# Optimization experiments

Measured on AMD Instinct MI355X. Metric: run time of the kernel, lower is better.

Reference implementation:

```python
import jax, jax.numpy as jnp
import numpy as np

L = 5          # num_layer
D = 128        # emb_dim
F = 16         # raw node/edge feature dim
N = 50000      # nodes
E = 800000     # edges
BN_EPS = 1e-5


def _bn(z, g, b):
    # BatchNorm1d forward with batch statistics (training-mode math)
    m = z.mean(axis=0)
    v = z.var(axis=0)
    return (z - m) * jax.lax.rsqrt(v + BN_EPS) * g + b


def setup_inputs() -> dict:
    key = jax.random.key(0)
    ks = jax.random.split(key, 8)
    s = lambda *sh: 0.05  # weight scale
    return {
        "x": jax.random.normal(ks[0], (N, F), jnp.float32),
        "edge_index": jax.random.randint(ks[1], (2, E), 0, N, jnp.int32),
        "edge_attr": jax.random.normal(ks[2], (E, F), jnp.float32),
        "W_node": jax.random.normal(ks[3], (F, D), jnp.float32) * 0.05,
        "b_node": jnp.zeros((D,), jnp.float32),
        "We": jax.random.normal(ks[4], (L, F, D), jnp.float32) * 0.05,
        "be": jnp.zeros((L, D), jnp.float32),
        "eps_gin": jnp.zeros((L,), jnp.float32),
        "W1": jax.random.normal(ks[5], (L, D, 2 * D), jnp.float32) * 0.05,
        "b1": jnp.zeros((L, 2 * D), jnp.float32),
        "g1": jnp.ones((L, 2 * D), jnp.float32),
        "beta1": jnp.zeros((L, 2 * D), jnp.float32),
        "W2": jax.random.normal(ks[6], (L, 2 * D, D), jnp.float32) * 0.05,
        "b2": jnp.zeros((L, D), jnp.float32),
        "g_bn": jnp.ones((L, D), jnp.float32),
        "beta_bn": jnp.zeros((L, D), jnp.float32),
    }


def reference(x, edge_index, edge_attr, W_node, b_node, We, be, eps_gin,
              W1, b1, g1, beta1, W2, b2, g_bn, beta_bn):
    src, dst = edge_index[0], edge_index[1]
    n = x.shape[0]
    h = x @ W_node + b_node                       # node encoder: [N, D]
    for l in range(L):
        e = edge_attr @ We[l] + be[l]             # edge encoder: [E, D]
        msg = jax.nn.relu(h[src] + e)             # gather + message
        agg = jax.ops.segment_sum(msg, dst, num_segments=n)  # scatter-add
        z = (1.0 + eps_gin[l]) * h + agg
        z = _bn(z @ W1[l] + b1[l], g1[l], beta1[l])  # GIN MLP hidden
        z = jax.nn.relu(z)
        z = z @ W2[l] + b2[l]                     # GIN MLP out: [N, D]
        z = _bn(z, g_bn[l], beta_bn[l])           # per-layer BatchNorm
        if l < L - 1:
            z = jax.nn.relu(z)                    # dropout is identity (p=0)
        h = z + h                                 # residual
    return h                                      # JK = 'last'
```

## Files before the change

kernel.cpp:

```cpp
#include <hip/hip_runtime.h>
#include <hip/hip_bf16.h>

#define NN 50000
#define EE 800000
#define DD 128
#define FF 16
#define LL 5
#define NPART 3125

typedef __attribute__((ext_vector_type(8))) short bf16x8;
typedef __attribute__((ext_vector_type(4))) float f32x4;

__device__ __forceinline__ unsigned short f2bf(float f) {
    union { float f; unsigned int u; } v; v.f = f;
    unsigned int u = v.u;
    unsigned int r = (u + 0x7fffu + ((u >> 16) & 1u)) >> 16;
    return (unsigned short)r;
}
__device__ __forceinline__ float bf2f(unsigned short s) {
    union { unsigned int u; float f; } v; v.u = ((unsigned int)s) << 16;
    return v.f;
}

__global__ void k_node_enc(const float* __restrict__ x, const float* __restrict__ Wn,
                           const float* __restrict__ bn, float* __restrict__ h)
{
    const int t = blockIdx.x * 256 + threadIdx.x;
    const int i = t >> 7, d = t & 127;
    const float4* x4 = (const float4*)(x + (size_t)i * 16);
    float4 a0 = x4[0], a1 = x4[1], a2 = x4[2], a3 = x4[3];
    float acc = bn[d];
    acc += a0.x*Wn[0*128+d] + a0.y*Wn[1*128+d] + a0.z*Wn[2*128+d] + a0.w*Wn[3*128+d];
    acc += a1.x*Wn[4*128+d] + a1.y*Wn[5*128+d] + a1.z*Wn[6*128+d] + a1.w*Wn[7*128+d];
    acc += a2.x*Wn[8*128+d] + a2.y*Wn[9*128+d] + a2.z*Wn[10*128+d] + a2.w*Wn[11*128+d];
    acc += a3.x*Wn[12*128+d] + a3.y*Wn[13*128+d] + a3.z*Wn[14*128+d] + a3.w*Wn[15*128+d];
    h[t] = acc;
}

__global__ void k_count(const int* __restrict__ ei, int* __restrict__ counts)
{
    const int e = blockIdx.x * 256 + threadIdx.x;
    atomicAdd(&counts[ei[EE + e]], 1);
}

__global__ __launch_bounds__(1024) void k_scan(int* __restrict__ counts, int* __restrict__ row_ptr)
{
    __shared__ int wsum[16];
    __shared__ int carry;
    const int tid = threadIdx.x, lane = tid & 63, w = tid >> 6;
    if (tid == 0) carry = 0;
    __syncthreads();
    for (int base = 0; base < NN; base += 1024) {
        const int i = base + tid;
        const int v = (i < NN) ? counts[i] : 0;
        int x = v;
        #pragma unroll
        for (int off = 1; off < 64; off <<= 1) {
            const int t = __shfl_up(x, off);
            if (lane >= off) x += t;
        }
        if (lane == 63) wsum[w] = x;
        __syncthreads();
        int woff = 0, total = 0;
        #pragma unroll
        for (int j = 0; j < 16; ++j) { const int s = wsum[j]; total += s; if (j < w) woff += s; }
        const int ex = carry + woff + x - v;
        if (i < NN) { row_ptr[i] = ex; counts[i] = ex; }
        __syncthreads();
        if (tid == 0) carry += total;
        __syncthreads();
    }
    if (tid == 0) row_ptr[NN] = carry;
}

__global__ void k_fill(const int* __restrict__ ei, int* __restrict__ cursor, int2* __restrict__ eidsrc)
{
    const int e = blockIdx.x * 256 + threadIdx.x;
    const int d = ei[EE + e];
    const int p = atomicAdd(&cursor[d], 1);
    eidsrc[p] = make_int2(e, ei[e]);
}

__global__ void k_pack(const float* __restrict__ W1, const float* __restrict__ W2,
                       unsigned short* __restrict__ Wp1, unsigned short* __restrict__ Wp2)
{
    int t = blockIdx.x * 256 + threadIdx.x;
    const int total = LL * 32768;
    if (t < total) {
        const int l = t >> 15, r = t & 32767;
        const int j = r & 7, lane = (r >> 3) & 63, kt = (r >> 9) & 3, nt = r >> 11;
        const int k = kt * 32 + (lane >> 4) * 8 + j;
        const int n = nt * 16 + (lane & 15);
        Wp1[t] = f2bf(W1[(size_t)l * 32768 + k * 256 + n]);
    } else {
        t -= total;
        const int l = t >> 15, r = t & 32767;
        const int j = r & 7, lane = (r >> 3) & 63, kt = (r >> 9) & 7, nt = r >> 12;
        const int k = kt * 32 + (lane >> 4) * 8 + j;
        const int n = nt * 16 + (lane & 15);
        Wp2[t] = f2bf(W2[(size_t)l * 32768 + k * 128 + n]);
    }
}

__global__ __launch_bounds__(256) void k_agg(
    const float* __restrict__ h, const float* __restrict__ ea,
    const float* __restrict__ We_l, const float* __restrict__ be_l,
    const int* __restrict__ row_ptr, const int2* __restrict__ eidsrc,
    float* __restrict__ agg)
{
    const int wv = threadIdx.x >> 6;
    const int v  = blockIdx.x * 4 + wv;
    const int lane = threadIdx.x & 63;
    const int c2 = lane * 2;
    float2 w[16];
    #pragma unroll
    for (int f = 0; f < 16; ++f) w[f] = *(const float2*)(We_l + f * 128 + c2);
    const float2 bed = *(const float2*)(be_l + c2);
    const int kbeg = __builtin_amdgcn_readfirstlane(row_ptr[v]);
    const int kend = __builtin_amdgcn_readfirstlane(row_ptr[v + 1]);
    float2 acc0 = {0.f, 0.f}, acc1 = {0.f, 0.f}, acc2 = {0.f, 0.f}, acc3 = {0.f, 0.f};

#define EDGE_DOT(eidx_, hs_, out_) do {                                        \
        const float4* p_ = (const float4*)(ea + (size_t)(eidx_) * 16);         \
        const float4 a0_ = p_[0], a1_ = p_[1], a2_ = p_[2], a3_ = p_[3];       \
        float ex_ = bed.x, ey_ = bed.y;                                        \
        ex_ += a0_.x*w[0].x  + a0_.y*w[1].x  + a0_.z*w[2].x  + a0_.w*w[3].x;   \
        ey_ += a0_.x*w[0].y  + a0_.y*w[1].y  + a0_.z*w[2].y  + a0_.w*w[3].y;   \
        ex_ += a1_.x*w[4].x  + a1_.y*w[5].x  + a1_.z*w[6].x  + a1_.w*w[7].x;   \
        ey_ += a1_.x*w[4].y  + a1_.y*w[5].y  + a1_.z*w[6].y  + a1_.w*w[7].y;   \
        ex_ += a2_.x*w[8].x  + a2_.y*w[9].x  + a2_.z*w[10].x + a2_.w*w[11].x;  \
        ey_ += a2_.x*w[8].y  + a2_.y*w[9].y  + a2_.z*w[10].y + a2_.w*w[11].y;  \
        ex_ += a3_.x*w[12].x + a3_.y*w[13].x + a3_.z*w[14].x + a3_.w*w[15].x;  \
        ey_ += a3_.x*w[12].y + a3_.y*w[13].y + a3_.z*w[14].y + a3_.w*w[15].y;  \
        const float mx_ = hs_.x + ex_, my_ = hs_.y + ey_;                      \
        (out_).x += mx_ > 0.f ? mx_ : 0.f;                                     \
        (out_).y += my_ > 0.f ? my_ : 0.f;                                     \
    } while (0)

    int k = kbeg;
    int2 q0, q1, q2, q3;
    bool have = (k + 4 <= kend);
    if (have) { q0 = eidsrc[k]; q1 = eidsrc[k+1]; q2 = eidsrc[k+2]; q3 = eidsrc[k+3]; }
    while (have) {
        const int e0 = __builtin_amdgcn_readfirstlane(q0.x);
        const int s0 = __builtin_amdgcn_readfirstlane(q0.y);
        const int e1 = __builtin_amdgcn_readfirstlane(q1.x);
        const int s1 = __builtin_amdgcn_readfirstlane(q1.y);
        const int e2 = __builtin_amdgcn_readfirstlane(q2.x);
        const int s2 = __builtin_amdgcn_readfirstlane(q2.y);
        const int e3 = __builtin_amdgcn_readfirstlane(q3.x);
        const int s3 = __builtin_amdgcn_readfirstlane(q3.y);
        const float2 h0 = *(const float2*)(h + (size_t)s0 * 128 + c2);
        const float2 h1 = *(const float2*)(h + (size_t)s1 * 128 + c2);
        const float2 h2 = *(const float2*)(h + (size_t)s2 * 128 + c2);
        const float2 h3 = *(const float2*)(h + (size_t)s3 * 128 + c2);
        const int kn = k + 4;
        const bool haven = (kn + 4 <= kend);
        int2 n0, n1, n2, n3;
        if (haven) { n0 = eidsrc[kn]; n1 = eidsrc[kn+1]; n2 = eidsrc[kn+2]; n3 = eidsrc[kn+3]; }
        EDGE_DOT(e0, h0, acc0);
        EDGE_DOT(e1, h1, acc1);
        EDGE_DOT(e2, h2, acc2);
        EDGE_DOT(e3, h3, acc3);
        q0 = n0; q1 = n1; q2 = n2; q3 = n3;
        k = kn; have = haven;
    }
    for (; k < kend; ++k) {
        const int2 q = eidsrc[k];
        const int e0 = __builtin_amdgcn_readfirstlane(q.x);
        const int s0 = __builtin_amdgcn_readfirstlane(q.y);
        const float2 h0 = *(const float2*)(h + (size_t)s0 * 128 + c2);
        EDGE_DOT(e0, h0, acc0);
    }
#undef EDGE_DOT
    float2 r;
    r.x = (acc0.x + acc1.x) + (acc2.x + acc3.x);
    r.y = (acc0.y + acc1.y) + (acc2.y + acc3.y);
    *(float2*)(agg + (size_t)v * 128 + c2) = r;
}

__global__ __launch_bounds__(256) void k_gemmB(
    const float* __restrict__ h, const float* __restrict__ agg,
    const float* __restrict__ eps_gin, const int l,
    const unsigned short* __restrict__ Wp,
    unsigned short* __restrict__ t_bf,
    float* __restrict__ ps, float* __restrict__ pq)
{
    __shared__ __align__(16) unsigned short zs[16 * 136];
    const int tid = threadIdx.x;
    const int r0 = blockIdx.x * 16;
    const float epsv = 1.0f + eps_gin[l];
    {
        const int row = tid & 15, c0 = (tid >> 4) * 8;
        const float4* hp = (const float4*)(h   + (size_t)(r0 + row) * 128 + c0);
        const float4* ap = (const float4*)(agg + (size_t)(r0 + row) * 128 + c0);
        const float4 h0 = hp[0], h1 = hp[1], a0 = ap[0], a1 = ap[1];
        union { bf16x8 v; unsigned short u[8]; } pk;
        pk.u[0] = f2bf(epsv*h0.x + a0.x);
        pk.u[1] = f2bf(epsv*h0.y + a0.y);
        pk.u[2] = f2bf(epsv*h0.z + a0.z);
        pk.u[3] = f2bf(epsv*h0.w + a0.w);
        pk.u[4] = f2bf(epsv*h1.x + a1.x);
        pk.u[5] = f2bf(epsv*h1.y + a1.y);
        pk.u[6] = f2bf(epsv*h1.z + a1.z);
        pk.u[7] = f2bf(epsv*h1.w + a1.w);
        *(bf16x8*)(&zs[row * 136 + c0]) = pk.v;
    }
    __syncthreads();
    const int w = tid >> 6, l6 = tid & 63, m = l6 & 15, quad = l6 >> 4;
    const f32x4 z4 = {0.f, 0.f, 0.f, 0.f};
    f32x4 acc[4] = {z4, z4, z4, z4};
    const bf16x8* Wv = (const bf16x8*)Wp;
    #pragma unroll
    for (int kt = 0; kt < 4; ++kt) {
        const bf16x8 a = *(const bf16x8*)(&zs[m * 136 + kt * 32 + quad * 8]);
        #pragma unroll
        for (int f = 0; f < 4; ++f) {
            const bf16x8 b = Wv[((w * 4 + f) * 4 + kt) * 64 + l6];
            acc[f] = __builtin_amdgcn_mfma_f32_16x16x32_bf16(a, b, acc[f], 0, 0, 0);
        }
    }
    const int rowb = r0 + quad * 4;
    #pragma unroll
    for (int f = 0; f < 4; ++f) {
        const int col = w * 64 + f * 16 + m;
        float ssum = 0.f, ssq = 0.f;
        #pragma unroll
        for (int r = 0; r < 4; ++r) {
            const float val = acc[f][r];
            t_bf[(size_t)(rowb + r) * 256 + col] = f2bf(val);
            ssum += val; ssq += val * val;
        }
        ssum += __shfl_xor(ssum, 16); ssum += __shfl_xor(ssum, 32);
        ssq  += __shfl_xor(ssq , 16); ssq  += __shfl_xor(ssq , 32);
        if (quad == 0) {
            ps[(size_t)col * NPART + blockIdx.x] = ssum;
            pq[(size_t)col * NPART + blockIdx.x] = ssq;
        }
    }
}

__global__ void k_bnstat(const float* __restrict__ ps, const float* __restrict__ pq,
                         const float* __restrict__ g, const float* __restrict__ beta,
                         float* __restrict__ sc, float* __restrict__ sh)
{
    const int c = blockIdx.x;
    const int tid = threadIdx.x;
    const float* pr = ps + (size_t)c * NPART;
    const float* qr = pq + (size_t)c * NPART;
    float s = 0.f, q = 0.f;
    for (int i = tid; i < NPART; i += 256) { s += pr[i]; q += qr[i]; }
    #pragma unroll
    for (int off = 1; off < 64; off <<= 1) { s += __shfl_xor(s, off); q += __shfl_xor(q, off); }
    __shared__ float ls[4], lq[4];
    const int wv = tid >> 6;
    if ((tid & 63) == 0) { ls[wv] = s; lq[wv] = q; }
    __syncthreads();
    if (tid == 0) {
        const float S = ls[0] + ls[1] + ls[2] + ls[3];
        const float Q = lq[0] + lq[1] + lq[2] + lq[3];
        const float mean = S * (1.0f / NN);
        const float var  = Q * (1.0f / NN) - mean * mean;
        const float rs = rsqrtf(var + 1e-5f);
        const float scale = g[c] * rs;
        sc[c] = scale;
        sh[c] = beta[c] - mean * scale;
    }
}

__global__ __launch_bounds__(128) void k_gemmD(
    const unsigned short* __restrict__ t_bf,
    const float* __restrict__ sc1, const float* __restrict__ sh1,
    const unsigned short* __restrict__ Wp,
    float* __restrict__ vbuf,
    float* __restrict__ ps, float* __restrict__ pq)
{
    __shared__ __align__(16) unsigned short us[16 * 264];
    const int tid = threadIdx.x;
    const int r0 = blockIdx.x * 16;
    {
        const int row = tid & 15, g8 = (tid >> 4) * 8;
        #pragma unroll
        for (int cc = 0; cc < 4; ++cc) {
            const int c = cc * 64 + g8;
            union { bf16x8 v; unsigned short u[8]; } in, o;
            in.v = *(const bf16x8*)(t_bf + (size_t)(r0 + row) * 256 + c);
            const float4* scp = (const float4*)(sc1 + c);
            const float4* shp = (const float4*)(sh1 + c);
            const float4 s0 = scp[0], s1 = scp[1], b0 = shp[0], b1 = shp[1];
            float xv;
            xv = bf2f(in.u[0])*s0.x + b0.x; o.u[0] = f2bf(xv > 0.f ? xv : 0.f);
            xv = bf2f(in.u[1])*s0.y + b0.y; o.u[1] = f2bf(xv > 0.f ? xv : 0.f);
            xv = bf2f(in.u[2])*s0.z + b0.z; o.u[2] = f2bf(xv > 0.f ? xv : 0.f);
            xv = bf2f(in.u[3])*s0.w + b0.w; o.u[3] = f2bf(xv > 0.f ? xv : 0.f);
            xv = bf2f(in.u[4])*s1.x + b1.x; o.u[4] = f2bf(xv > 0.f ? xv : 0.f);
            xv = bf2f(in.u[5])*s1.y + b1.y; o.u[5] = f2bf(xv > 0.f ? xv : 0.f);
            xv = bf2f(in.u[6])*s1.z + b1.z; o.u[6] = f2bf(xv > 0.f ? xv : 0.f);
            xv = bf2f(in.u[7])*s1.w + b1.w; o.u[7] = f2bf(xv > 0.f ? xv : 0.f);
            *(bf16x8*)(&us[row * 264 + c]) = o.v;
        }
    }
    __syncthreads();
    const int w = tid >> 6, l6 = tid & 63, m = l6 & 15, quad = l6 >> 4;
    const f32x4 z4 = {0.f, 0.f, 0.f, 0.f};
    f32x4 acc[4] = {z4, z4, z4, z4};
    const bf16x8* Wv = (const bf16x8*)Wp;
    #pragma unroll
    for (int kt = 0; kt < 8; ++kt) {
        const bf16x8 a = *(const bf16x8*)(&us[m * 264 + kt * 32 + quad * 8]);
        #pragma unroll
        for (int f = 0; f < 4; ++f) {
            const bf16x8 b = Wv[((w * 4 + f) * 8 + kt) * 64 + l6];
            acc[f] = __builtin_amdgcn_mfma_f32_16x16x32_bf16(a, b, acc[f], 0, 0, 0);
        }
    }
    const int rowb = r0 + quad * 4;
    #pragma unroll
    for (int f = 0; f < 4; ++f) {
        const int col = w * 64 + f * 16 + m;
        float ssum = 0.f, ssq = 0.f;
        #pragma unroll
        for (int r = 0; r < 4; ++r) {
            const float val = acc[f][r];
            vbuf[(size_t)(rowb + r) * 128 + col] = val;
            ssum += val; ssq += val * val;
        }
        ssum += __shfl_xor(ssum, 16); ssum += __shfl_xor(ssum, 32);
        ssq  += __shfl_xor(ssq , 16); ssq  += __shfl_xor(ssq , 32);
        if (quad == 0) {
            ps[(size_t)col * NPART + blockIdx.x] = ssum;
            pq[(size_t)col * NPART + blockIdx.x] = ssq;
        }
    }
}

__global__ void k_fin(const float* __restrict__ vbuf, const float* __restrict__ sc2,
                      const float* __restrict__ sh2, float* __restrict__ h, const int do_relu)
{
    const int t = blockIdx.x * 256 + threadIdx.x;
    const int c = t & 127;
    float z = vbuf[t] * sc2[c] + sh2[c];
    if (do_relu) z = z > 0.f ? z : 0.f;
    h[t] += z;
}

extern "C" void kernel_launch(void* const* d_in, const int* in_sizes, int n_in,
                              void* d_out, int out_size, void* d_ws, size_t ws_size,
                              hipStream_t stream)
{
    const float* x       = (const float*)d_in[0];
    const int*   ei      = (const int*)  d_in[1];
    const float* ea      = (const float*)d_in[2];
    const float* W_node  = (const float*)d_in[3];
    const float* b_node  = (const float*)d_in[4];
    const float* We      = (const float*)d_in[5];
    const float* be      = (const float*)d_in[6];
    const float* eps_gin = (const float*)d_in[7];
    const float* W1      = (const float*)d_in[8];
    const float* g1      = (const float*)d_in[10];
    const float* beta1   = (const float*)d_in[11];
    const float* W2      = (const float*)d_in[12];
    const float* g_bn    = (const float*)d_in[14];
    const float* beta_bn = (const float*)d_in[15];

    float* h = (float*)d_out;

    char* W = (char*)d_ws;
    int*   counts  = (int*)  (W + 0);
    int*   row_ptr = (int*)  (W + 200000);
    float* sc1     = (float*)(W + 400016);
    float* sh1     = (float*)(W + 401040);
    float* sc2     = (float*)(W + 402064);
    float* sh2     = (float*)(W + 402576);
    float* ps1     = (float*)(W + 403088);
    float* pq1     = (float*)(W + 3603088);
    float* ps2     = (float*)(W + 6803088);
    float* pq2     = (float*)(W + 8403088);
    int2*  eidsrc  = (int2*) (W + 10003088);
    unsigned short* Wp1 = (unsigned short*)(W + 16403088);
    unsigned short* Wp2 = (unsigned short*)(W + 16730768);
    float* agg     = (float*)(W + 17058448);
    unsigned short* t_bf = (unsigned short*)(W + 42658448);
    float* vbuf    = (float*)(W + 68258448);

    (void)hipMemsetAsync(counts, 0, 200000, stream);

    k_node_enc<<<dim3(NN * DD / 256), dim3(256), 0, stream>>>(x, W_node, b_node, h);
    k_count<<<dim3(EE / 256), dim3(256), 0, stream>>>(ei, counts);
    k_scan<<<dim3(1), dim3(1024), 0, stream>>>(counts, row_ptr);
    k_fill<<<dim3(EE / 256), dim3(256), 0, stream>>>(ei, counts, eidsrc);
    k_pack<<<dim3(2 * LL * 32768 / 256), dim3(256), 0, stream>>>(W1, W2, Wp1, Wp2);

    for (int l = 0; l < LL; ++l) {
        k_agg<<<dim3(NN / 4), dim3(256), 0, stream>>>(
            h, ea, We + (size_t)l * FF * DD, be + (size_t)l * DD, row_ptr, eidsrc, agg);
        k_gemmB<<<dim3(NPART), dim3(256), 0, stream>>>(
            h, agg, eps_gin, l, Wp1 + (size_t)l * 32768, t_bf, ps1, pq1);
        k_bnstat<<<dim3(256), dim3(256), 0, stream>>>(
            ps1, pq1, g1 + (size_t)l * 256, beta1 + (size_t)l * 256, sc1, sh1);
        k_gemmD<<<dim3(NPART), dim3(128), 0, stream>>>(
            t_bf, sc1, sh1, Wp2 + (size_t)l * 32768, vbuf, ps2, pq2);
        k_bnstat<<<dim3(128), dim3(256), 0, stream>>>(
            ps2, pq2, g_bn + (size_t)l * 128, beta_bn + (size_t)l * 128, sc2, sh2);
        k_fin<<<dim3(NN * DD / 256), dim3(256), 0, stream>>>(vbuf, sc2, sh2, h, (l < LL - 1) ? 1 : 0);
    }
}
```

Before: 1.053 ms.

## Store activations and edge features in bf16 and fuse GIN combine into aggregation

After: 949.9 us. -9.8%, faster.

```diff
diff --git a/kernel.cpp b/kernel.cpp
--- a/kernel.cpp
+++ b/kernel.cpp
@@ -21,9 +21,12 @@
     union { unsigned int u; float f; } v; v.u = ((unsigned int)s) << 16;
     return v.f;
 }
+#define BFLO(u) __uint_as_float((unsigned int)(u) << 16)
+#define BFHI(u) __uint_as_float((unsigned int)(u) & 0xffff0000u)
 
 __global__ void k_node_enc(const float* __restrict__ x, const float* __restrict__ Wn,
-                           const float* __restrict__ bn, float* __restrict__ h)
+                           const float* __restrict__ bn, float* __restrict__ h,
+                           unsigned short* __restrict__ h_bf)
 {
     const int t = blockIdx.x * 256 + threadIdx.x;
     const int i = t >> 7, d = t & 127;
@@ -35,6 +38,7 @@
     acc += a2.x*Wn[8*128+d] + a2.y*Wn[9*128+d] + a2.z*Wn[10*128+d] + a2.w*Wn[11*128+d];
     acc += a3.x*Wn[12*128+d] + a3.y*Wn[13*128+d] + a3.z*Wn[14*128+d] + a3.w*Wn[15*128+d];
     h[t] = acc;
+    h_bf[t] = f2bf(acc);
 }
 
 __global__ void k_count(const int* __restrict__ ei, int* __restrict__ counts)
@@ -73,12 +77,23 @@
     if (tid == 0) row_ptr[NN] = carry;
 }
 
-__global__ void k_fill(const int* __restrict__ ei, int* __restrict__ cursor, int2* __restrict__ eidsrc)
+__global__ void k_fill(const int* __restrict__ ei, const float* __restrict__ ea,
+                       int* __restrict__ cursor, int* __restrict__ src_perm,
+                       unsigned short* __restrict__ ea_bf)
 {
     const int e = blockIdx.x * 256 + threadIdx.x;
-    const int d = ei[EE + e];
-    const int p = atomicAdd(&cursor[d], 1);
-    eidsrc[p] = make_int2(e, ei[e]);
+    const int dst = ei[EE + e];
+    const int p = atomicAdd(&cursor[dst], 1);
+    src_perm[p] = ei[e];
+    const float4* s4 = (const float4*)(ea + (size_t)e * 16);
+    const float4 a0 = s4[0], a1 = s4[1], a2 = s4[2], a3 = s4[3];
+    union { bf16x8 v; unsigned short u[8]; } o0, o1;
+    o0.u[0]=f2bf(a0.x); o0.u[1]=f2bf(a0.y); o0.u[2]=f2bf(a0.z); o0.u[3]=f2bf(a0.w);
+    o0.u[4]=f2bf(a1.x); o0.u[5]=f2bf(a1.y); o0.u[6]=f2bf(a1.z); o0.u[7]=f2bf(a1.w);
+    o1.u[0]=f2bf(a2.x); o1.u[1]=f2bf(a2.y); o1.u[2]=f2bf(a2.z); o1.u[3]=f2bf(a2.w);
+    o1.u[4]=f2bf(a3.x); o1.u[5]=f2bf(a3.y); o1.u[6]=f2bf(a3.z); o1.u[7]=f2bf(a3.w);
+    bf16x8* dp = (bf16x8*)(ea_bf + (size_t)p * 16);
+    dp[0] = o0.v; dp[1] = o1.v;
 }
 
 __global__ void k_pack(const float* __restrict__ W1, const float* __restrict__ W2,
@@ -103,10 +118,11 @@
 }
 
 __global__ __launch_bounds__(256) void k_agg(
-    const float* __restrict__ h, const float* __restrict__ ea,
+    const unsigned short* __restrict__ h_bf, const unsigned short* __restrict__ ea_bf,
     const float* __restrict__ We_l, const float* __restrict__ be_l,
-    const int* __restrict__ row_ptr, const int2* __restrict__ eidsrc,
-    float* __restrict__ agg)
+    const float* __restrict__ eps_gin, const int l,
+    const int* __restrict__ row_ptr, const int* __restrict__ src_perm,
+    unsigned short* __restrict__ z_bf)
 {
     const int wv = threadIdx.x >> 6;
     const int v  = blockIdx.x * 4 + wv;
@@ -116,72 +132,80 @@
     #pragma unroll
     for (int f = 0; f < 16; ++f) w[f] = *(const float2*)(We_l + f * 128 + c2);
     const float2 bed = *(const float2*)(be_l + c2);
+    const float epsv = 1.0f + eps_gin[l];
     const int kbeg = __builtin_amdgcn_readfirstlane(row_ptr[v]);
     const int kend = __builtin_amdgcn_readfirstlane(row_ptr[v + 1]);
-    float2 acc0 = {0.f, 0.f}, acc1 = {0.f, 0.f}, acc2 = {0.f, 0.f}, acc3 = {0.f, 0.f};
-
-#define EDGE_DOT(eidx_, hs_, out_) do {                                        \
-        const float4* p_ = (const float4*)(ea + (size_t)(eidx_) * 16);         \
-        const float4 a0_ = p_[0], a1_ = p_[1], a2_ = p_[2], a3_ = p_[3];       \
-        float ex_ = bed.x, ey_ = bed.y;                                        \
-        ex_ += a0_.x*w[0].x  + a0_.y*w[1].x  + a0_.z*w[2].x  + a0_.w*w[3].x;   \
-        ey_ += a0_.x*w[0].y  + a0_.y*w[1].y  + a0_.z*w[2].y  + a0_.w*w[3].y;   \
-        ex_ += a1_.x*w[4].x  + a1_.y*w[5].x  + a1_.z*w[6].x  + a1_.w*w[7].x;   \
-        ey_ += a1_.x*w[4].y  + a1_.y*w[5].y  + a1_.z*w[6].y  + a1_.w*w[7].y;   \
-        ex_ += a2_.x*w[8].x  + a2_.y*w[9].x  + a2_.z*w[10].x + a2_.w*w[11].x;  \
-        ey_ += a2_.x*w[8].y  + a2_.y*w[9].y  + a2_.z*w[10].y + a2_.w*w[11].y;  \
-        ex_ += a3_.x*w[12].x + a3_.y*w[13].x + a3_.z*w[14].x + a3_.w*w[15].x;  \
-        ey_ += a3_.x*w[12].y + a3_.y*w[13].y + a3_.z*w[14].y + a3_.w*w[15].y;  \
-        const float mx_ = hs_.x + ex_, my_ = hs_.y + ey_;                      \
-        (out_).x += mx_ > 0.f ? mx_ : 0.f;                                     \
-        (out_).y += my_ > 0.f ? my_ : 0.f;                                     \
+    float2 acc0 = {0.f,0.f}, acc1 = {0.f,0.f}, acc2 = {0.f,0.f}, acc3 = {0.f,0.f};
+
+#define LOAD_GROUP(kk, S0,S1,S2,S3, E0,E1,E2,E3,E4,E5,E6,E7, H0,H1,H2,H3)  \
+    { const int* sp_ = src_perm + (kk);                                     \
+      S0 = __builtin_amdgcn_readfirstlane(sp_[0]);                          \
+      S1 = __builtin_amdgcn_readfirstlane(sp_[1]);                          \
+      S2 = __builtin_amdgcn_readfirstlane(sp_[2]);                          \
+      S3 = __builtin_amdgcn_readfirstlane(sp_[3]);                          \
+      const uint4* ep_ = (const uint4*)(ea_bf + (size_t)(kk) * 16);         \
+      E0 = ep_[0]; E1 = ep_[1]; E2 = ep_[2]; E3 = ep_[3];                   \
+      E4 = ep_[4]; E5 = ep_[5]; E6 = ep_[6]; E7 = ep_[7];                   \
+      H0 = *(const unsigned int*)(h_bf + (size_t)S0 * 128 + c2);            \
+      H1 = *(const unsigned int*)(h_bf + (size_t)S1 * 128 + c2);            \
+      H2 = *(const unsigned int*)(h_bf + (size_t)S2 * 128 + c2);            \
+      H3 = *(const unsigned int*)(h_bf + (size_t)S3 * 128 + c2); }
+
+#define EDGE_DOT(EA, EB, HQ, OUT) do {                                      \
+        float ex_ = bed.x, ey_ = bed.y, a_;                                 \
+        a_ = BFLO(EA.x); ex_ += a_*w[0].x;  ey_ += a_*w[0].y;               \
+        a_ = BFHI(EA.x); ex_ += a_*w[1].x;  ey_ += a_*w[1].y;               \
+        a_ = BFLO(EA.y); ex_ += a_*w[2].x;  ey_ += a_*w[2].y;               \
+        a_ = BFHI(EA.y); ex_ += a_*w[3].x;  ey_ += a_*w[3].y;               \
+        a_ = BFLO(EA.z); ex_ += a_*w[4].x;  ey_ += a_*w[4].y;               \
+        a_ = BFHI(EA.z); ex_ += a_*w[5].x;  ey_ += a_*w[5].y;               \
+        a_ = BFLO(EA.w); ex_ += a_*w[6].x;  ey_ += a_*w[6].y;               \
+        a_ = BFHI(EA.w); ex_ += a_*w[7].x;  ey_ += a_*w[7].y;               \
+        a_ = BFLO(EB.x); ex_ += a_*w[8].x;  ey_ += a_*w[8].y;               \
+        a_ = BFHI(EB.x); ex_ += a_*w[9].x;  ey_ += a_*w[9].y;               \
+        a_ = BFLO(EB.y); ex_ += a_*w[10].x; ey_ += a_*w[10].y;              \
+        a_ = BFHI(EB.y); ex_ += a_*w[11].x; ey_ += a_*w[11].y;              \
+        a_ = BFLO(EB.z); ex_ += a_*w[12].x; ey_ += a_*w[12].y;              \
+        a_ = BFHI(EB.z); ex_ += a_*w[13].x; ey_ += a_*w[13].y;              \
+        a_ = BFLO(EB.w); ex_ += a_*w[14].x; ey_ += a_*w[14].y;              \
+        a_ = BFHI(EB.w); ex_ += a_*w[15].x; ey_ += a_*w[15].y;              \
+        const float mx_ = BFLO(HQ) + ex_, my_ = BFHI(HQ) + ey_;             \
+        OUT.x += mx_ > 0.f ? mx_ : 0.f;                                     \
+        OUT.y += my_ > 0.f ? my_ : 0.f;                                     \
     } while (0)
 
     int k = kbeg;
-    int2 q0, q1, q2, q3;
-    bool have = (k + 4 <= kend);
-    if (have) { q0 = eidsrc[k]; q1 = eidsrc[k+1]; q2 = eidsrc[k+2]; q3 = eidsrc[k+3]; }
-    while (have) {
-        const int e0 = __builtin_amdgcn_readfirstlane(q0.x);
-        const int s0 = __builtin_amdgcn_readfirstlane(q0.y);
-        const int e1 = __builtin_amdgcn_readfirstlane(q1.x);
-        const int s1 = __builtin_amdgcn_readfirstlane(q1.y);
-        const int e2 = __builtin_amdgcn_readfirstlane(q2.x);
-        const int s2 = __builtin_amdgcn_readfirstlane(q2.y);
-        const int e3 = __builtin_amdgcn_readfirstlane(q3.x);
-        const int s3 = __builtin_amdgcn_readfirstlane(q3.y);
-        const float2 h0 = *(const float2*)(h + (size_t)s0 * 128 + c2);
-        const float2 h1 = *(const float2*)(h + (size_t)s1 * 128 + c2);
-        const float2 h2 = *(const float2*)(h + (size_t)s2 * 128 + c2);
-        const float2 h3 = *(const float2*)(h + (size_t)s3 * 128 + c2);
-        const int kn = k + 4;
-        const bool haven = (kn + 4 <= kend);
-        int2 n0, n1, n2, n3;
-        if (haven) { n0 = eidsrc[kn]; n1 = eidsrc[kn+1]; n2 = eidsrc[kn+2]; n3 = eidsrc[kn+3]; }
-        EDGE_DOT(e0, h0, acc0);
-        EDGE_DOT(e1, h1, acc1);
-        EDGE_DOT(e2, h2, acc2);
-        EDGE_DOT(e3, h3, acc3);
-        q0 = n0; q1 = n1; q2 = n2; q3 = n3;
-        k = kn; have = haven;
-    }
-    for (; k < kend; ++k) {
-        const int2 q = eidsrc[k];
-        const int e0 = __builtin_amdgcn_readfirstlane(q.x);
-        const int s0 = __builtin_amdgcn_readfirstlane(q.y);
-        const float2 h0 = *(const float2*)(h + (size_t)s0 * 128 + c2);
-        EDGE_DOT(e0, h0, acc0);
+    int cs0, cs1, cs2, cs3;
+    uint4 ce0, ce1, ce2, ce3, ce4, ce5, ce6, ce7;
+    unsigned int ch0, ch1, ch2, ch3;
+    if (k < kend) {
+        LOAD_GROUP(k, cs0,cs1,cs2,cs3, ce0,ce1,ce2,ce3,ce4,ce5,ce6,ce7, ch0,ch1,ch2,ch3);
+    }
+    for (; k < kend; k += 4) {
+        int ns0, ns1, ns2, ns3;
+        uint4 ne0, ne1, ne2, ne3, ne4, ne5, ne6, ne7;
+        unsigned int nh0, nh1, nh2, nh3;
+        LOAD_GROUP(k + 4, ns0,ns1,ns2,ns3, ne0,ne1,ne2,ne3,ne4,ne5,ne6,ne7, nh0,nh1,nh2,nh3);
+        EDGE_DOT(ce0, ce1, ch0, acc0);
+        if (k + 1 < kend) EDGE_DOT(ce2, ce3, ch1, acc1);
+        if (k + 2 < kend) EDGE_DOT(ce4, ce5, ch2, acc2);
+        if (k + 3 < kend) EDGE_DOT(ce6, ce7, ch3, acc3);
+        cs0=ns0; cs1=ns1; cs2=ns2; cs3=ns3;
+        ce0=ne0; ce1=ne1; ce2=ne2; ce3=ne3; ce4=ne4; ce5=ne5; ce6=ne6; ce7=ne7;
+        ch0=nh0; ch1=nh1; ch2=nh2; ch3=nh3;
     }
 #undef EDGE_DOT
-    float2 r;
-    r.x = (acc0.x + acc1.x) + (acc2.x + acc3.x);
-    r.y = (acc0.y + acc1.y) + (acc2.y + acc3.y);
-    *(float2*)(agg + (size_t)v * 128 + c2) = r;
+#undef LOAD_GROUP
+    (void)cs0; (void)cs1; (void)cs2; (void)cs3;
+    const unsigned int hv = *(const unsigned int*)(h_bf + (size_t)v * 128 + c2);
+    const float zx = epsv * BFLO(hv) + ((acc0.x + acc1.x) + (acc2.x + acc3.x));
+    const float zy = epsv * BFHI(hv) + ((acc0.y + acc1.y) + (acc2.y + acc3.y));
+    const unsigned int zp = (unsigned int)f2bf(zx) | ((unsigned int)f2bf(zy) << 16);
+    *(unsigned int*)(z_bf + (size_t)v * 128 + c2) = zp;
 }
 
 __global__ __launch_bounds__(256) void k_gemmB(
-    const float* __restrict__ h, const float* __restrict__ agg,
-    const float* __restrict__ eps_gin, const int l,
+    const unsigned short* __restrict__ z_bf,
     const unsigned short* __restrict__ Wp,
     unsigned short* __restrict__ t_bf,
     float* __restrict__ ps, float* __restrict__ pq)
@@ -189,22 +213,10 @@
     __shared__ __align__(16) unsigned short zs[16 * 136];
     const int tid = threadIdx.x;
     const int r0 = blockIdx.x * 16;
-    const float epsv = 1.0f + eps_gin[l];
     {
         const int row = tid & 15, c0 = (tid >> 4) * 8;
-        const float4* hp = (const float4*)(h   + (size_t)(r0 + row) * 128 + c0);
-        const float4* ap = (const float4*)(agg + (size_t)(r0 + row) * 128 + c0);
-        const float4 h0 = hp[0], h1 = hp[1], a0 = ap[0], a1 = ap[1];
-        union { bf16x8 v; unsigned short u[8]; } pk;
-        pk.u[0] = f2bf(epsv*h0.x + a0.x);
-        pk.u[1] = f2bf(epsv*h0.y + a0.y);
-        pk.u[2] = f2bf(epsv*h0.z + a0.z);
-        pk.u[3] = f2bf(epsv*h0.w + a0.w);
-        pk.u[4] = f2bf(epsv*h1.x + a1.x);
-        pk.u[5] = f2bf(epsv*h1.y + a1.y);
-        pk.u[6] = f2bf(epsv*h1.z + a1.z);
-        pk.u[7] = f2bf(epsv*h1.w + a1.w);
-        *(bf16x8*)(&zs[row * 136 + c0]) = pk.v;
+        *(bf16x8*)(&zs[row * 136 + c0]) =
+            *(const bf16x8*)(z_bf + (size_t)(r0 + row) * 128 + c0);
     }
     __syncthreads();
     const int w = tid >> 6, l6 = tid & 63, m = l6 & 15, quad = l6 >> 4;
@@ -272,7 +284,7 @@
     const unsigned short* __restrict__ t_bf,
     const float* __restrict__ sc1, const float* __restrict__ sh1,
     const unsigned short* __restrict__ Wp,
-    float* __restrict__ vbuf,
+    unsigned short* __restrict__ vb,
     float* __restrict__ ps, float* __restrict__ pq)
 {
     __shared__ __align__(16) unsigned short us[16 * 264];
@@ -322,7 +334,7 @@
         #pragma unroll
         for (int r = 0; r < 4; ++r) {
             const float val = acc[f][r];
-            vbuf[(size_t)(rowb + r) * 128 + col] = val;
+            vb[(size_t)(rowb + r) * 128 + col] = f2bf(val);
             ssum += val; ssq += val * val;
         }
         ssum += __shfl_xor(ssum, 16); ssum += __shfl_xor(ssum, 32);
@@ -334,14 +346,33 @@
     }
 }
 
-__global__ void k_fin(const float* __restrict__ vbuf, const float* __restrict__ sc2,
-                      const float* __restrict__ sh2, float* __restrict__ h, const int do_relu)
+__global__ void k_fin(const unsigned short* __restrict__ vb,
+                      const float* __restrict__ sc2, const float* __restrict__ sh2,
+                      float* __restrict__ h, unsigned short* __restrict__ h_bf,
+                      const int do_relu)
 {
     const int t = blockIdx.x * 256 + threadIdx.x;
-    const int c = t & 127;
-    float z = vbuf[t] * sc2[c] + sh2[c];
-    if (do_relu) z = z > 0.f ? z : 0.f;
-    h[t] += z;
+    const int base = t * 8;
+    const int c = base & 127;
+    union { bf16x8 v; unsigned short u[8]; } in, ob;
+    in.v = *(const bf16x8*)(vb + base);
+    const float4 s0 = *(const float4*)(sc2 + c), s1 = *(const float4*)(sc2 + c + 4);
+    const float4 b0 = *(const float4*)(sh2 + c), b1 = *(const float4*)(sh2 + c + 4);
+    float4 h0 = *(const float4*)(h + base), h1 = *(const float4*)(h + base + 4);
+    float z;
+    z = bf2f(in.u[0])*s0.x + b0.x; if (do_relu) z = z > 0.f ? z : 0.f; h0.x += z;
+    z = bf2f(in.u[1])*s0.y + b0.y; if (do_relu) z = z > 0.f ? z : 0.f; h0.y += z;
+    z = bf2f(in.u[2])*s0.z + b0.z; if (do_relu) z = z > 0.f ? z : 0.f; h0.z += z;
+    z = bf2f(in.u[3])*s0.w + b0.w; if (do_relu) z = z > 0.f ? z : 0.f; h0.w += z;
+    z = bf2f(in.u[4])*s1.x + b1.x; if (do_relu) z = z > 0.f ? z : 0.f; h1.x += z;
+    z = bf2f(in.u[5])*s1.y + b1.y; if (do_relu) z = z > 0.f ? z : 0.f; h1.y += z;
+    z = bf2f(in.u[6])*s1.z + b1.z; if (do_relu) z = z > 0.f ? z : 0.f; h1.z += z;
+    z = bf2f(in.u[7])*s1.w + b1.w; if (do_relu) z = z > 0.f ? z : 0.f; h1.w += z;
+    *(float4*)(h + base) = h0;
+    *(float4*)(h + base + 4) = h1;
+    ob.u[0]=f2bf(h0.x); ob.u[1]=f2bf(h0.y); ob.u[2]=f2bf(h0.z); ob.u[3]=f2bf(h0.w);
+    ob.u[4]=f2bf(h1.x); ob.u[5]=f2bf(h1.y); ob.u[6]=f2bf(h1.z); ob.u[7]=f2bf(h1.w);
+    *(bf16x8*)(h_bf + base) = ob.v;
 }
 
 extern "C" void kernel_launch(void* const* d_in, const int* in_sizes, int n_in,
@@ -366,42 +397,47 @@
     float* h = (float*)d_out;
 
     char* W = (char*)d_ws;
-    int*   counts  = (int*)  (W + 0);
-    int*   row_ptr = (int*)  (W + 200000);
-    float* sc1     = (float*)(W + 400016);
-    float* sh1     = (float*)(W + 401040);
-    float* sc2     = (float*)(W + 402064);
-    float* sh2     = (float*)(W + 402576);
-    float* ps1     = (float*)(W + 403088);
-    float* pq1     = (float*)(W + 3603088);
-    float* ps2     = (float*)(W + 6803088);
-    float* pq2     = (float*)(W + 8403088);
-    int2*  eidsrc  = (int2*) (W + 10003088);
-    unsigned short* Wp1 = (unsigned short*)(W + 16403088);
-    unsigned short* Wp2 = (unsigned short*)(W + 16730768);
-    float* agg     = (float*)(W + 17058448);
-    unsigned short* t_bf = (unsigned short*)(W + 42658448);
-    float* vbuf    = (float*)(W + 68258448);
+    int*   counts   = (int*)  (W + 0);
+    int*   row_ptr  = (int*)  (W + 200000);
+    float* sc1      = (float*)(W + 400016);
+    float* sh1      = (float*)(W + 401040);
+    float* sc2      = (float*)(W + 402064);
+    float* sh2      = (float*)(W + 402576);
+    float* ps1      = (float*)(W + 403088);
+    float* pq1      = (float*)(W + 3603088);
+    float* ps2      = (float*)(W + 6803088);
+    float* pq2      = (float*)(W + 8403088);
+    int*   src_perm = (int*)  (W + 10003088);
+    unsigned short* ea_bf = (unsigned short*)(W + 13203120);
+    unsigned short* Wp1   = (unsigned short*)(W + 38803376);
+    unsigned short* Wp2   = (unsigned short*)(W + 39131056);
+    unsigned short* z_bf  = (unsigned short*)(W + 39458736);
+    unsigned short* t_bf  = (unsigned short*)(W + 52258736);
+    unsigned short* h_bf  = (unsigned short*)(W + 77858736);
+    unsigned short* vb    = z_bf;
 
     (void)hipMemsetAsync(counts, 0, 200000, stream);
-
-    k_node_enc<<<dim3(NN * DD / 256), dim3(256), 0, stream>>>(x, W_node, b_node, h);
+    (void)hipMemsetAsync(src_perm + EE, 0, 32, stream);
+
+    k_node_enc<<<dim3(NN * DD / 256), dim3(256), 0, stream>>>(x, W_node, b_node, h, h_bf);
     k_count<<<dim3(EE / 256), dim3(256), 0, stream>>>(ei, counts);
     k_scan<<<dim3(1), dim3(1024), 0, stream>>>(counts, row_ptr);
-    k_fill<<<dim3(EE / 256), dim3(256), 0, stream>>>(ei, counts, eidsrc);
+    k_fill<<<dim3(EE / 256), dim3(256), 0, stream>>>(ei, ea, counts, src_perm, ea_bf);
     k_pack<<<dim3(2 * LL * 32768 / 256), dim3(256), 0, stream>>>(W1, W2, Wp1, Wp2);
 
     for (int l = 0; l < LL; ++l) {
         k_agg<<<dim3(NN / 4), dim3(256), 0, stream>>>(
-            h, ea, We + (size_t)l * FF * DD, be + (size_t)l * DD, row_ptr, eidsrc, agg);
+            h_bf, ea_bf, We + (size_t)l * FF * DD, be + (size_t)l * DD,
+            eps_gin, l, row_ptr, src_perm, z_bf);
         k_gemmB<<<dim3(NPART), dim3(256), 0, stream>>>(
-            h, agg, eps_gin, l, Wp1 + (size_t)l * 32768, t_bf, ps1, pq1);
+            z_bf, Wp1 + (size_t)l * 32768, t_bf, ps1, pq1);
         k_bnstat<<<dim3(256), dim3(256), 0, stream>>>(
             ps1, pq1, g1 + (size_t)l * 256, beta1 + (size_t)l * 256, sc1, sh1);
         k_gemmD<<<dim3(NPART), dim3(128), 0, stream>>>(
-            t_bf, sc1, sh1, Wp2 + (size_t)l * 32768, vbuf, ps2, pq2);
+            t_bf, sc1, sh1, Wp2 + (size_t)l * 32768, vb, ps2, pq2);
         k_bnstat<<<dim3(128), dim3(256), 0, stream>>>(
             ps2, pq2, g_bn + (size_t)l * 128, beta_bn + (size_t)l * 128, sc2, sh2);
-        k_fin<<<dim3(NN * DD / 256), dim3(256), 0, stream>>>(vbuf, sc2, sh2, h, (l < LL - 1) ? 1 : 0);
-    }
-}
+        k_fin<<<dim3(NN * DD / 8 / 256), dim3(256), 0, stream>>>(
+            vb, sc2, sh2, h, h_bf, (l < LL - 1) ? 1 : 0);
+    }
+}
```
